# Optimization experiments

Measured on AMD Instinct MI355X. Metric: run time of the kernel, lower is better.

## Reference

```python
import jax, jax.numpy as jnp
import numpy as np

B, N, Mdim, CS, INP, OUT = 256, 2048, 64, 512, 256, 256
ADDR_R = Mdim + 6          # k(M), beta(1), g(1), s(3), gamma(1)
ADDR_W = 3 * Mdim + 6      # + erase(M) + add(M)


def setup_inputs() -> dict:
    key = jax.random.key(0)
    ks = jax.random.split(key, 16)
    s = 0.05
    x = jax.random.normal(ks[0], (B, INP), dtype=jnp.float32)
    memory = jax.random.uniform(ks[1], (B, N, Mdim), dtype=jnp.float32) * 0.1 + 1e-6
    h = jax.random.normal(ks[2], (B, CS), dtype=jnp.float32) * 0.1
    c = jax.random.normal(ks[3], (B, CS), dtype=jnp.float32) * 0.1
    rw = jax.random.uniform(ks[4], (B, N), dtype=jnp.float32)
    read_w = rw / rw.sum(axis=1, keepdims=True)
    ww = jax.random.uniform(ks[5], (B, N), dtype=jnp.float32)
    write_w = ww / ww.sum(axis=1, keepdims=True)
    prev_read = jax.random.normal(ks[6], (B, Mdim), dtype=jnp.float32) * 0.1
    W_ih = jax.random.normal(ks[7], (4 * CS, INP + Mdim), dtype=jnp.float32) * s
    W_hh = jax.random.normal(ks[8], (4 * CS, CS), dtype=jnp.float32) * s
    b_ih = jnp.zeros((4 * CS,), jnp.float32)
    b_hh = jnp.zeros((4 * CS,), jnp.float32)
    W_r = jax.random.normal(ks[9], (ADDR_R, CS), dtype=jnp.float32) * s
    b_r = jnp.zeros((ADDR_R,), jnp.float32)
    W_w = jax.random.normal(ks[10], (ADDR_W, CS), dtype=jnp.float32) * s
    b_w = jnp.zeros((ADDR_W,), jnp.float32)
    W_o = jax.random.normal(ks[11], (OUT, CS + Mdim), dtype=jnp.float32) * s
    b_o = jnp.zeros((OUT,), jnp.float32)
    return dict(x=x, memory=memory, h=h, c=c, read_w=read_w, write_w=write_w,
                prev_read=prev_read, W_ih=W_ih, W_hh=W_hh, b_ih=b_ih, b_hh=b_hh,
                W_r=W_r, b_r=b_r, W_w=W_w, b_w=b_w, W_o=W_o, b_o=b_o)


def _addressing(out_vec, prev_w, memory, M):
    # Eq. 5-9: content softmax, interpolation, circular shift, sharpening.
    k = out_vec[:, :M]                                   # [B, M]
    beta = jax.nn.softplus(out_vec[:, M:M + 1])          # [B, 1]
    g = jax.nn.sigmoid(out_vec[:, M + 1:M + 2])          # [B, 1]
    s = jax.nn.softmax(out_vec[:, M + 2:M + 5], axis=1)  # [B, 3]
    gamma = 1.0 + jax.nn.softplus(out_vec[:, M + 5:M + 6])
    norm_k = jnp.linalg.norm(k, axis=1, keepdims=True) + 1e-8        # [B, 1]
    norm_mem = jnp.linalg.norm(memory, axis=2) + 1e-8                # [B, N]
    sim = jnp.einsum('bnm,bm->bn', memory, k) / (norm_k * norm_mem)  # cosine
    w_c = jax.nn.softmax(beta * sim, axis=1)
    w_g = g * w_c + (1.0 - g) * prev_w
    # circular convolution with 3-tap shift kernel (replaces the roll loop)
    w_s = (s[:, 0:1] * jnp.roll(w_g, 1, axis=1)
           + s[:, 1:2] * w_g
           + s[:, 2:3] * jnp.roll(w_g, -1, axis=1))
    w_pow = w_s ** gamma
    return w_pow / (w_pow.sum(axis=1, keepdims=True) + 1e-8)


def reference(x, memory, h, c, read_w, write_w, prev_read,
              W_ih, W_hh, b_ih, b_hh, W_r, b_r, W_w, b_w, W_o, b_o):
    M = memory.shape[2]
    inp = jnp.concatenate([x, prev_read], axis=1)
    gates = inp @ W_ih.T + b_ih + h @ W_hh.T + b_hh
    i_g, f_g, g_g, o_g = jnp.split(gates, 4, axis=1)  # torch LSTMCell gate order
    i_g = jax.nn.sigmoid(i_g); f_g = jax.nn.sigmoid(f_g)
    g_g = jnp.tanh(g_g); o_g = jax.nn.sigmoid(o_g)
    c_new = f_g * c + i_g * g_g
    h_new = o_g * jnp.tanh(c_new)
    # read head (uses pre-write memory)
    read_out = h_new @ W_r.T + b_r
    w_read = _addressing(read_out, read_w, memory, M)
    read_vec = jnp.einsum('bn,bnm->bm', w_read, memory)
    # write head: address, then erase/add outer-product update
    write_out = h_new @ W_w.T + b_w
    w_write = _addressing(write_out, write_w, memory, M)
    erase = jax.nn.sigmoid(write_out[:, M + 6:2 * M + 6])
    add = write_out[:, 2 * M + 6:3 * M + 6]
    memory_new = memory * (1.0 - w_write[:, :, None] * erase[:, None, :]) \
                 + w_write[:, :, None] * add[:, None, :]
    out = jnp.concatenate([h_new, read_vec], axis=1) @ W_o.T + b_o
    return (out, memory_new, h_new, c_new, w_read, w_write, read_vec)
```

## Files before the change

### kernel.cpp

```cpp
#include <hip/hip_runtime.h>
#include <math.h>

#define Bsz   256
#define Nn    2048
#define Md    64
#define CSd   512
#define INPd  256
#define OUTd  256
#define KTOT  832
#define PSTRIDE 272
#define GSZ   524288

__device__ __forceinline__ float sigmoidf_(float x){ return 1.f/(1.f+expf(-x)); }
__device__ __forceinline__ float softplusf_(float x){ return fmaxf(x,0.f) + log1pf(expf(-fabsf(x))); }

__global__ __launch_bounds__(256) void k_gates(
    const float* __restrict__ x, const float* __restrict__ prev_read, const float* __restrict__ h,
    const float* __restrict__ W_ih, const float* __restrict__ W_hh,
    float* __restrict__ partials)
{
  __shared__ __align__(16) float As[16][34];
  __shared__ __align__(16) float Bs[16][68];
  const int t = threadIdx.x;
  const int col0 = blockIdx.x * 64;
  const int row0 = blockIdx.y * 32;
  const int z    = blockIdx.z;
  const int tx = t & 15;
  const int ty = t >> 4;
  const int arow = t >> 3;
  const int ak   = (t & 7) * 2;
  const int bcol = t >> 2;
  const int bk   = (t & 3) * 4;
  const int grow = row0 + arow;
  const int j    = col0 + bcol;

  float acc[2][4] = {};
  for (int kc = 0; kc < 13; ++kc) {
    const int kbase = z * 208 + kc * 16;
    #pragma unroll
    for (int i = 0; i < 2; ++i) {
      int k = kbase + ak + i;
      float v;
      if (k < INPd)            v = x[grow*INPd + k];
      else if (k < INPd+Md)    v = prev_read[grow*Md + (k-INPd)];
      else                     v = h[grow*CSd + (k-INPd-Md)];
      As[ak+i][arow] = v;
    }
    {
      int k = kbase + bk;
      float4 wv;
      if (k < INPd+Md) wv = *(const float4*)&W_ih[j*(INPd+Md) + k];
      else             wv = *(const float4*)&W_hh[j*CSd + (k-INPd-Md)];
      Bs[bk+0][bcol] = wv.x; Bs[bk+1][bcol] = wv.y;
      Bs[bk+2][bcol] = wv.z; Bs[bk+3][bcol] = wv.w;
    }
    __syncthreads();
    #pragma unroll
    for (int kk = 0; kk < 16; ++kk) {
      float2 av = *(const float2*)&As[kk][ty*2];
      float4 bv = *(const float4*)&Bs[kk][tx*4];
      acc[0][0] += av.x*bv.x; acc[0][1] += av.x*bv.y;
      acc[0][2] += av.x*bv.z; acc[0][3] += av.x*bv.w;
      acc[1][0] += av.y*bv.x; acc[1][1] += av.y*bv.y;
      acc[1][2] += av.y*bv.z; acc[1][3] += av.y*bv.w;
    }
    __syncthreads();
  }
  float* part = partials + (size_t)z * GSZ;
  #pragma unroll
  for (int i = 0; i < 2; ++i) {
    float4 v = {acc[i][0], acc[i][1], acc[i][2], acc[i][3]};
    *(float4*)&part[(row0 + ty*2 + i)*2048 + col0 + tx*4] = v;
  }
}

__global__ __launch_bounds__(256) void k_lstm(const float* __restrict__ partials,
    const float* __restrict__ c, const float* __restrict__ b_ih, const float* __restrict__ b_hh,
    float* __restrict__ h_new, float* __restrict__ c_new)
{
  int idx = blockIdx.x*256 + threadIdx.x;
  int b = idx >> 9, jj = idx & 511;
  float g[4];
  #pragma unroll
  for (int q = 0; q < 4; ++q) {
    int col = q*512 + jj;
    float s = b_ih[col] + b_hh[col];
    #pragma unroll
    for (int sp = 0; sp < 4; ++sp) s += partials[(size_t)sp*GSZ + b*2048 + col];
    g[q] = s;
  }
  float ig = sigmoidf_(g[0]);
  float fg = sigmoidf_(g[1]);
  float gg = tanhf(g[2]);
  float og = sigmoidf_(g[3]);
  float cn = fg * c[idx] + ig * gg;
  c_new[idx] = cn;
  h_new[idx] = og * tanhf(cn);
}

__global__ __launch_bounds__(512) void k_heads(
    const float* __restrict__ h_new,
    const float* __restrict__ W_r, const float* __restrict__ b_r,
    const float* __restrict__ W_w, const float* __restrict__ b_w,
    float* __restrict__ params)
{
  __shared__ float hs[CSd];
  __shared__ float ob[268];
  int b = blockIdx.x, t = threadIdx.x;
  hs[t] = h_new[b*CSd + t];
  __syncthreads();
  int wave = t >> 6, lane = t & 63;
  for (int r = wave; r < 268; r += 8) {
    const float* wrow; float bias;
    if (r < 70) { wrow = W_r + r*CSd;      bias = b_r[r]; }
    else        { wrow = W_w + (r-70)*CSd; bias = b_w[r-70]; }
    float s = 0.f;
    #pragma unroll
    for (int i = 0; i < 8; ++i) s += wrow[i*64 + lane] * hs[i*64 + lane];
    #pragma unroll
    for (int off = 32; off; off >>= 1) s += __shfl_xor(s, off);
    if (lane == 0) ob[r] = s + bias;
  }
  __syncthreads();
  float* P = params + b*PSTRIDE;
  if (t < 256) {
    if (t < 64)       P[t] = ob[t];
    else if (t < 128) P[t] = ob[70 + (t-64)];
    else if (t < 192) P[t] = sigmoidf_(ob[140 + (t-128)]);
    else              P[t] = ob[204 + (t-192)];
  }
  float* S = P + 256;
  if (wave == 0) {
    float v = ob[lane]; float sq = v*v;
    #pragma unroll
    for (int off = 32; off; off >>= 1) sq += __shfl_xor(sq, off);
    if (lane == 0) S[6] = 1.f/(sqrtf(sq)+1e-8f);
  } else if (wave == 1) {
    float v = ob[70 + lane]; float sq = v*v;
    #pragma unroll
    for (int off = 32; off; off >>= 1) sq += __shfl_xor(sq, off);
    if (lane == 0) S[13] = 1.f/(sqrtf(sq)+1e-8f);
  }
  if (t == 128) {
    S[0] = softplusf_(ob[64]);
    S[1] = sigmoidf_(ob[65]);
    float m3 = fmaxf(ob[66], fmaxf(ob[67], ob[68]));
    float e0=expf(ob[66]-m3), e1=expf(ob[67]-m3), e2=expf(ob[68]-m3);
    float es = e0+e1+e2;
    S[2]=e0/es; S[3]=e1/es; S[4]=e2/es;
    S[5] = 1.f + softplusf_(ob[69]);
  }
  if (t == 129) {
    S[7] = softplusf_(ob[134]);
    S[8] = sigmoidf_(ob[135]);
    float m3 = fmaxf(ob[136], fmaxf(ob[137], ob[138]));
    float e0=expf(ob[136]-m3), e1=expf(ob[137]-m3), e2=expf(ob[138]-m3);
    float es = e0+e1+e2;
    S[9]=e0/es; S[10]=e1/es; S[11]=e2/es;
    S[12] = 1.f + softplusf_(ob[139]);
  }
}

__global__ __launch_bounds__(256) void k_sim(
    const float* __restrict__ mem, const float* __restrict__ params,
    float* __restrict__ a_r, float* __restrict__ a_w)
{
  int b = blockIdx.y;
  int n = blockIdx.x*16 + (threadIdx.x >> 4);
  int chunk = threadIdx.x & 15;
  float4 v = ((const float4*)mem)[(b*Nn + n)*16 + chunk];
  const float* P = params + b*PSTRIDE;
  float4 kr = ((const float4*)P)[chunk];
  float4 kw = ((const float4*)(P+64))[chunk];
  float ss = v.x*v.x + v.y*v.y + v.z*v.z + v.w*v.w;
  float pr = v.x*kr.x + v.y*kr.y + v.z*kr.z + v.w*kr.w;
  float pw = v.x*kw.x + v.y*kw.y + v.z*kw.z + v.w*kw.w;
  #pragma unroll
  for (int off=8; off; off>>=1) {
    ss += __shfl_xor(ss, off);
    pr += __shfl_xor(pr, off);
    pw += __shfl_xor(pw, off);
  }
  if (chunk == 0) {
    float inv_nm = 1.f/(sqrtf(ss)+1e-8f);
    const float* S = P + 256;
    a_r[b*Nn+n] = S[0] * pr * S[6]  * inv_nm;
    a_w[b*Nn+n] = S[7] * pw * S[13] * inv_nm;
  }
}

__device__ __forceinline__ float block_reduce512(float val, float* red, int t, bool ismax){
  #pragma unroll
  for (int off=32; off; off>>=1)
    val = ismax ? fmaxf(val, __shfl_xor(val,off)) : val + __shfl_xor(val,off);
  __syncthreads();
  if ((t&63)==0) red[t>>6] = val;
  __syncthreads();
  float r = red[0];
  if (ismax) { for (int i=1;i<8;++i) r = fmaxf(r, red[i]); }
  else       { for (int i=1;i<8;++i) r += red[i]; }
  return r;
}

__global__ __launch_bounds__(512) void k_weights(
    const float* __restrict__ a_r, const float* __restrict__ a_w,
    const float* __restrict__ read_w, const float* __restrict__ write_w,
    const float* __restrict__ params,
    float* __restrict__ w_read, float* __restrict__ w_write)
{
  __shared__ float wg[Nn];
  __shared__ float red[8];
  int b = blockIdx.x;
  int which = blockIdx.y;
  const float* a    = which ? a_w     : a_r;
  const float* prev = which ? write_w : read_w;
  float* outw       = which ? w_write : w_read;
  const float* S = params + b*PSTRIDE + 256 + (which ? 7 : 0);
  float g = S[1], s0 = S[2], s1 = S[3], s2 = S[4], gamma = S[5];
  int t = threadIdx.x;
  float v[4];
  #pragma unroll
  for (int i=0;i<4;++i) v[i] = a[b*Nn + t*4+i];
  float lmax = fmaxf(fmaxf(v[0],v[1]), fmaxf(v[2],v[3]));
  float mx = block_reduce512(lmax, red, t, true);
  float e[4]; float ps = 0.f;
  #pragma unroll
  for (int i=0;i<4;++i){ e[i] = expf(v[i]-mx); ps += e[i]; }
  float denom = block_reduce512(ps, red, t, false);
  float inv = 1.f/denom;
  #pragma unroll
  for (int i=0;i<4;++i){
    float wc = e[i]*inv;
    wg[t*4+i] = g*wc + (1.f-g)*prev[b*Nn + t*4+i];
  }
  __syncthreads();
  float wp[4]; float psum = 0.f;
  #pragma unroll
  for (int i=0;i<4;++i){
    int n = t*4+i;
    float wsv = s0*wg[(n+Nn-1)&(Nn-1)] + s1*wg[n] + s2*wg[(n+1)&(Nn-1)];
    wp[i] = powf(wsv, gamma);
    psum += wp[i];
  }
  float tot = block_reduce512(psum, red, t, false);
  float invt = 1.f/(tot + 1e-8f);
  #pragma unroll
  for (int i=0;i<4;++i) outw[b*Nn + t*4+i] = wp[i]*invt;
}

__global__ __launch_bounds__(256) void k_memupd(
    const float* __restrict__ mem, const float* __restrict__ params,
    const float* __restrict__ w_read, const float* __restrict__ w_write,
    float* __restrict__ mem_new, float* __restrict__ read_vec)
{
  __shared__ __align__(16) float er[64];
  __shared__ __align__(16) float ad[64];
  __shared__ float4 part[64];
  int b = blockIdx.y;
  int n0 = blockIdx.x * 64;
  int t = threadIdx.x;
  const float* P = params + b*PSTRIDE;
  if (t < 64)       er[t]    = P[128+t];
  else if (t < 128) ad[t-64] = P[192+(t-64)];
  __syncthreads();
  int chunk = t & 15;
  int rr = t >> 4;
  float4 e4 = ((const float4*)er)[chunk];
  float4 a4 = ((const float4*)ad)[chunk];
  float4 acc = {0.f,0.f,0.f,0.f};
  #pragma unroll
  for (int p = 0; p < 4; ++p) {
    int n = n0 + p*16 + rr;
    float4 v = ((const float4*)mem)[(b*Nn+n)*16 + chunk];
    float ww = w_write[b*Nn+n];
    float wr = w_read[b*Nn+n];
    float4 o;
    o.x = v.x*(1.f-ww*e4.x) + ww*a4.x;
    o.y = v.y*(1.f-ww*e4.y) + ww*a4.y;
    o.z = v.z*(1.f-ww*e4.z) + ww*a4.z;
    o.w = v.w*(1.f-ww*e4.w) + ww*a4.w;
    ((float4*)mem_new)[(b*Nn+n)*16 + chunk] = o;
    acc.x += wr*v.x; acc.y += wr*v.y; acc.z += wr*v.z; acc.w += wr*v.w;
  }
  #pragma unroll
  for (int off = 16; off <= 32; off <<= 1) {
    acc.x += __shfl_xor(acc.x, off);
    acc.y += __shfl_xor(acc.y, off);
    acc.z += __shfl_xor(acc.z, off);
    acc.w += __shfl_xor(acc.w, off);
  }
  int wave = t >> 6;
  int lane = t & 63;
  if (lane < 16) part[wave*16 + chunk] = acc;
  __syncthreads();
  if (t < 16) {
    float4 s = part[t];
    for (int w=1; w<4; ++w){ float4 q = part[w*16+t]; s.x+=q.x; s.y+=q.y; s.z+=q.z; s.w+=q.w; }
    atomicAdd(&read_vec[b*64 + t*4+0], s.x);
    atomicAdd(&read_vec[b*64 + t*4+1], s.y);
    atomicAdd(&read_vec[b*64 + t*4+2], s.z);
    atomicAdd(&read_vec[b*64 + t*4+3], s.w);
  }
}

__global__ __launch_bounds__(256) void k_out(
    const float* __restrict__ h_new, const float* __restrict__ read_vec,
    const float* __restrict__ W_o, const float* __restrict__ b_o,
    float* __restrict__ out)
{
  __shared__ float vbuf[576];
  int b = blockIdx.y, t = threadIdx.x;
  vbuf[t]     = h_new[b*CSd + t];
  vbuf[t+256] = h_new[b*CSd + t + 256];
  if (t < 64) vbuf[512+t] = read_vec[b*64 + t];
  __syncthreads();
  int wave = t >> 6, lane = t & 63;
  float vb[9];
  #pragma unroll
  for (int i = 0; i < 9; ++i) vb[i] = vbuf[i*64 + lane];
  int cbase = blockIdx.x*64 + wave*16;
  for (int jj = 0; jj < 16; ++jj) {
    int cc = cbase + jj;
    const float* w = W_o + cc*576;
    float s = 0.f;
    #pragma unroll
    for (int i = 0; i < 9; ++i) s += w[i*64 + lane] * vb[i];
    #pragma unroll
    for (int off = 32; off; off >>= 1) s += __shfl_xor(s, off);
    if (lane == 0) out[b*OUTd + cc] = s + b_o[cc];
  }
}

extern "C" void kernel_launch(void* const* d_in, const int* in_sizes, int n_in,
                              void* d_out, int out_size, void* d_ws, size_t ws_size,
                              hipStream_t stream)
{
  const float* x         = (const float*)d_in[0];
  const float* memory    = (const float*)d_in[1];
  const float* h         = (const float*)d_in[2];
  const float* c         = (const float*)d_in[3];
  const float* read_w    = (const float*)d_in[4];
  const float* write_w   = (const float*)d_in[5];
  const float* prev_read = (const float*)d_in[6];
  const float* W_ih      = (const float*)d_in[7];
  const float* W_hh      = (const float*)d_in[8];
  const float* b_ih      = (const float*)d_in[9];
  const float* b_hh      = (const float*)d_in[10];
  const float* W_r       = (const float*)d_in[11];
  const float* b_r       = (const float*)d_in[12];
  const float* W_w       = (const float*)d_in[13];
  const float* b_w       = (const float*)d_in[14];
  const float* W_o       = (const float*)d_in[15];
  const float* b_o       = (const float*)d_in[16];

  float* out      = (float*)d_out;
  float* mem_new  = out + 256*256;
  float* h_new    = mem_new + (size_t)256*2048*64;
  float* c_new    = h_new + 256*512;
  float* w_read   = c_new + 256*512;
  float* w_write  = w_read + 256*2048;
  float* read_vec = w_write + 256*2048;

  float* ws       = (float*)d_ws;
  float* params   = ws;
  float* partials = params + 256*PSTRIDE;
  float* a_r      = partials;
  float* a_w      = partials + GSZ;

  k_gates  <<<dim3(32,8,4), 256, 0, stream>>>(x, prev_read, h, W_ih, W_hh, partials);
  k_lstm   <<<512,          256, 0, stream>>>(partials, c, b_ih, b_hh, h_new, c_new);
  k_heads  <<<256,          512, 0, stream>>>(h_new, W_r, b_r, W_w, b_w, params);
  k_sim    <<<dim3(128,256),256, 0, stream>>>(memory, params, a_r, a_w);
  k_weights<<<dim3(256,2),  512, 0, stream>>>(a_r, a_w, read_w, write_w, params, w_read, w_write);
  hipMemsetAsync(read_vec, 0, 256*64*sizeof(float), stream);
  k_memupd <<<dim3(32,256), 256, 0, stream>>>(memory, params, w_read, w_write, mem_new, read_vec);
  k_out    <<<dim3(4,256),  256, 0, stream>>>(h_new, read_vec, W_o, b_o, out);
}
```

Measured before the change: 376.0 us.

## Retile gates GEMM, fuse LSTM with heads, replace read-vector atomics with partials

The gates GEMM now uses 64-thread blocks, each computing an 8x8 register tile per thread over a 64x64 output tile. It splits K eight ways and prefetches the next K slice into registers while the current one is being multiplied. The LSTM cell update is fused into the head-projection kernel, so h_new goes straight to shared memory and one launch plus a global round trip disappears. The read-vector atomics and their memset are replaced by per-block partial sums that k_out reduces. The cost is more workspace for eight split-K partials, and the fused kernel has to sum eight partials per gate.

```diff
diff --git a/kernel.cpp b/kernel.cpp
--- a/kernel.cpp
+++ b/kernel.cpp
@@ -10,104 +10,110 @@
 #define KTOT  832
 #define PSTRIDE 272
 #define GSZ   524288
+#define ZSPL  8
+#define KZ    104
 
 __device__ __forceinline__ float sigmoidf_(float x){ return 1.f/(1.f+expf(-x)); }
 __device__ __forceinline__ float softplusf_(float x){ return fmaxf(x,0.f) + log1pf(expf(-fabsf(x))); }
 
-__global__ __launch_bounds__(256) void k_gates(
+__device__ __forceinline__ float4 loadA4(const float* __restrict__ x, const float* __restrict__ pr,
+                                         const float* __restrict__ h, int row, int k){
+  if (k < INPd)            return *(const float4*)&x[row*INPd + k];
+  else if (k < INPd+Md)    return *(const float4*)&pr[row*Md + (k-INPd)];
+  else                     return *(const float4*)&h[row*CSd + (k-INPd-Md)];
+}
+__device__ __forceinline__ float4 loadW4(const float* __restrict__ Wih, const float* __restrict__ Whh,
+                                         int j, int k){
+  if (k < INPd+Md)         return *(const float4*)&Wih[j*(INPd+Md) + k];
+  else                     return *(const float4*)&Whh[j*CSd + (k-INPd-Md)];
+}
+
+__global__ __launch_bounds__(64) void k_gates(
     const float* __restrict__ x, const float* __restrict__ prev_read, const float* __restrict__ h,
     const float* __restrict__ W_ih, const float* __restrict__ W_hh,
     float* __restrict__ partials)
 {
-  __shared__ __align__(16) float As[16][34];
-  __shared__ __align__(16) float Bs[16][68];
+  __shared__ __align__(16) float As[8][68];
+  __shared__ __align__(16) float Bs[8][68];
   const int t = threadIdx.x;
   const int col0 = blockIdx.x * 64;
-  const int row0 = blockIdx.y * 32;
+  const int row0 = blockIdx.y * 64;
   const int z    = blockIdx.z;
-  const int tx = t & 15;
-  const int ty = t >> 4;
-  const int arow = t >> 3;
-  const int ak   = (t & 7) * 2;
-  const int bcol = t >> 2;
-  const int bk   = (t & 3) * 4;
-  const int grow = row0 + arow;
-  const int j    = col0 + bcol;
-
-  float acc[2][4] = {};
+  const int tr = t >> 3, tc = t & 7;
+  const int row = row0 + t;
+  const int j   = col0 + t;
+
+  float acc[8][8] = {};
+  float4 a0, a1, b0, b1;
+  int kb = z * KZ;
+  a0 = loadA4(x, prev_read, h, row, kb);   a1 = loadA4(x, prev_read, h, row, kb+4);
+  b0 = loadW4(W_ih, W_hh, j, kb);          b1 = loadW4(W_ih, W_hh, j, kb+4);
+
   for (int kc = 0; kc < 13; ++kc) {
-    const int kbase = z * 208 + kc * 16;
-    #pragma unroll
-    for (int i = 0; i < 2; ++i) {
-      int k = kbase + ak + i;
-      float v;
-      if (k < INPd)            v = x[grow*INPd + k];
-      else if (k < INPd+Md)    v = prev_read[grow*Md + (k-INPd)];
-      else                     v = h[grow*CSd + (k-INPd-Md)];
-      As[ak+i][arow] = v;
+    As[0][t]=a0.x; As[1][t]=a0.y; As[2][t]=a0.z; As[3][t]=a0.w;
+    As[4][t]=a1.x; As[5][t]=a1.y; As[6][t]=a1.z; As[7][t]=a1.w;
+    Bs[0][t]=b0.x; Bs[1][t]=b0.y; Bs[2][t]=b0.z; Bs[3][t]=b0.w;
+    Bs[4][t]=b1.x; Bs[5][t]=b1.y; Bs[6][t]=b1.z; Bs[7][t]=b1.w;
+    __syncthreads();
+    if (kc < 12) {
+      int kn = kb + (kc+1)*8;
+      a0 = loadA4(x, prev_read, h, row, kn);   a1 = loadA4(x, prev_read, h, row, kn+4);
+      b0 = loadW4(W_ih, W_hh, j, kn);          b1 = loadW4(W_ih, W_hh, j, kn+4);
     }
-    {
-      int k = kbase + bk;
-      float4 wv;
-      if (k < INPd+Md) wv = *(const float4*)&W_ih[j*(INPd+Md) + k];
-      else             wv = *(const float4*)&W_hh[j*CSd + (k-INPd-Md)];
-      Bs[bk+0][bcol] = wv.x; Bs[bk+1][bcol] = wv.y;
-      Bs[bk+2][bcol] = wv.z; Bs[bk+3][bcol] = wv.w;
+    #pragma unroll
+    for (int kk = 0; kk < 8; ++kk) {
+      float av[8], bv[8];
+      *(float4*)&av[0] = *(const float4*)&As[kk][tr*8];
+      *(float4*)&av[4] = *(const float4*)&As[kk][tr*8+4];
+      *(float4*)&bv[0] = *(const float4*)&Bs[kk][tc*8];
+      *(float4*)&bv[4] = *(const float4*)&Bs[kk][tc*8+4];
+      #pragma unroll
+      for (int i=0;i<8;++i)
+        #pragma unroll
+        for (int q=0;q<8;++q)
+          acc[i][q] += av[i]*bv[q];
     }
     __syncthreads();
-    #pragma unroll
-    for (int kk = 0; kk < 16; ++kk) {
-      float2 av = *(const float2*)&As[kk][ty*2];
-      float4 bv = *(const float4*)&Bs[kk][tx*4];
-      acc[0][0] += av.x*bv.x; acc[0][1] += av.x*bv.y;
-      acc[0][2] += av.x*bv.z; acc[0][3] += av.x*bv.w;
-      acc[1][0] += av.y*bv.x; acc[1][1] += av.y*bv.y;
-      acc[1][2] += av.y*bv.z; acc[1][3] += av.y*bv.w;
-    }
-    __syncthreads();
   }
   float* part = partials + (size_t)z * GSZ;
   #pragma unroll
-  for (int i = 0; i < 2; ++i) {
-    float4 v = {acc[i][0], acc[i][1], acc[i][2], acc[i][3]};
-    *(float4*)&part[(row0 + ty*2 + i)*2048 + col0 + tx*4] = v;
-  }
-}
-
-__global__ __launch_bounds__(256) void k_lstm(const float* __restrict__ partials,
-    const float* __restrict__ c, const float* __restrict__ b_ih, const float* __restrict__ b_hh,
-    float* __restrict__ h_new, float* __restrict__ c_new)
-{
-  int idx = blockIdx.x*256 + threadIdx.x;
-  int b = idx >> 9, jj = idx & 511;
+  for (int i=0;i<8;++i) {
+    int r = row0 + tr*8 + i;
+    float4 v0 = {acc[i][0],acc[i][1],acc[i][2],acc[i][3]};
+    float4 v1 = {acc[i][4],acc[i][5],acc[i][6],acc[i][7]};
+    *(float4*)&part[r*2048 + col0 + tc*8]     = v0;
+    *(float4*)&part[r*2048 + col0 + tc*8 + 4] = v1;
+  }
+}
+
+__global__ __launch_bounds__(512) void k_lstm_heads(
+    const float* __restrict__ partials, const float* __restrict__ c,
+    const float* __restrict__ b_ih, const float* __restrict__ b_hh,
+    const float* __restrict__ W_r, const float* __restrict__ b_r,
+    const float* __restrict__ W_w, const float* __restrict__ b_w,
+    float* __restrict__ h_new, float* __restrict__ c_new, float* __restrict__ params)
+{
+  __shared__ float hs[CSd];
+  __shared__ float ob[268];
+  int b = blockIdx.x, t = threadIdx.x;
   float g[4];
   #pragma unroll
   for (int q = 0; q < 4; ++q) {
-    int col = q*512 + jj;
+    int col = q*512 + t;
     float s = b_ih[col] + b_hh[col];
     #pragma unroll
-    for (int sp = 0; sp < 4; ++sp) s += partials[(size_t)sp*GSZ + b*2048 + col];
+    for (int sp = 0; sp < ZSPL; ++sp) s += partials[(size_t)sp*GSZ + b*2048 + col];
     g[q] = s;
   }
   float ig = sigmoidf_(g[0]);
   float fg = sigmoidf_(g[1]);
   float gg = tanhf(g[2]);
   float og = sigmoidf_(g[3]);
-  float cn = fg * c[idx] + ig * gg;
-  c_new[idx] = cn;
-  h_new[idx] = og * tanhf(cn);
-}
-
-__global__ __launch_bounds__(512) void k_heads(
-    const float* __restrict__ h_new,
-    const float* __restrict__ W_r, const float* __restrict__ b_r,
-    const float* __restrict__ W_w, const float* __restrict__ b_w,
-    float* __restrict__ params)
-{
-  __shared__ float hs[CSd];
-  __shared__ float ob[268];
-  int b = blockIdx.x, t = threadIdx.x;
-  hs[t] = h_new[b*CSd + t];
+  float cn = fg * c[b*CSd + t] + ig * gg;
+  float hn = og * tanhf(cn);
+  c_new[b*CSd + t] = cn;
+  h_new[b*CSd + t] = hn;
+  hs[t] = hn;
   __syncthreads();
   int wave = t >> 6, lane = t & 63;
   for (int r = wave; r < 268; r += 8) {
@@ -251,7 +257,7 @@
 __global__ __launch_bounds__(256) void k_memupd(
     const float* __restrict__ mem, const float* __restrict__ params,
     const float* __restrict__ w_read, const float* __restrict__ w_write,
-    float* __restrict__ mem_new, float* __restrict__ read_vec)
+    float* __restrict__ mem_new, float* __restrict__ prv)
 {
   __shared__ __align__(16) float er[64];
   __shared__ __align__(16) float ad[64];
@@ -290,29 +296,31 @@
     acc.w += __shfl_xor(acc.w, off);
   }
   int wave = t >> 6;
-  int lane = t & 63;
-  if (lane < 16) part[wave*16 + chunk] = acc;
+  if ((t & 63) < 16) part[wave*16 + chunk] = acc;
   __syncthreads();
   if (t < 16) {
     float4 s = part[t];
     for (int w=1; w<4; ++w){ float4 q = part[w*16+t]; s.x+=q.x; s.y+=q.y; s.z+=q.z; s.w+=q.w; }
-    atomicAdd(&read_vec[b*64 + t*4+0], s.x);
-    atomicAdd(&read_vec[b*64 + t*4+1], s.y);
-    atomicAdd(&read_vec[b*64 + t*4+2], s.z);
-    atomicAdd(&read_vec[b*64 + t*4+3], s.w);
+    *(float4*)&prv[(b*32 + blockIdx.x)*64 + t*4] = s;
   }
 }
 
 __global__ __launch_bounds__(256) void k_out(
-    const float* __restrict__ h_new, const float* __restrict__ read_vec,
+    const float* __restrict__ h_new, const float* __restrict__ prv,
     const float* __restrict__ W_o, const float* __restrict__ b_o,
-    float* __restrict__ out)
+    float* __restrict__ out, float* __restrict__ read_vec)
 {
   __shared__ float vbuf[576];
   int b = blockIdx.y, t = threadIdx.x;
   vbuf[t]     = h_new[b*CSd + t];
   vbuf[t+256] = h_new[b*CSd + t + 256];
-  if (t < 64) vbuf[512+t] = read_vec[b*64 + t];
+  if (t < 64) {
+    float s = 0.f;
+    #pragma unroll 8
+    for (int i = 0; i < 32; ++i) s += prv[(b*32 + i)*64 + t];
+    vbuf[512+t] = s;
+    if (blockIdx.x == 0) read_vec[b*64 + t] = s;
+  }
   __syncthreads();
   int wave = t >> 6, lane = t & 63;
   float vb[9];
@@ -366,13 +374,13 @@
   float* partials = params + 256*PSTRIDE;
   float* a_r      = partials;
   float* a_w      = partials + GSZ;
-
-  k_gates  <<<dim3(32,8,4), 256, 0, stream>>>(x, prev_read, h, W_ih, W_hh, partials);
-  k_lstm   <<<512,          256, 0, stream>>>(partials, c, b_ih, b_hh, h_new, c_new);
-  k_heads  <<<256,          512, 0, stream>>>(h_new, W_r, b_r, W_w, b_w, params);
-  k_sim    <<<dim3(128,256),256, 0, stream>>>(memory, params, a_r, a_w);
-  k_weights<<<dim3(256,2),  512, 0, stream>>>(a_r, a_w, read_w, write_w, params, w_read, w_write);
-  hipMemsetAsync(read_vec, 0, 256*64*sizeof(float), stream);
-  k_memupd <<<dim3(32,256), 256, 0, stream>>>(memory, params, w_read, w_write, mem_new, read_vec);
-  k_out    <<<dim3(4,256),  256, 0, stream>>>(h_new, read_vec, W_o, b_o, out);
-}
+  float* prv      = partials + 2*GSZ;
+
+  k_gates     <<<dim3(32,4,ZSPL), 64, 0, stream>>>(x, prev_read, h, W_ih, W_hh, partials);
+  k_lstm_heads<<<256,            512, 0, stream>>>(partials, c, b_ih, b_hh, W_r, b_r, W_w, b_w,
+                                                   h_new, c_new, params);
+  k_sim       <<<dim3(128,256),  256, 0, stream>>>(memory, params, a_r, a_w);
+  k_weights   <<<dim3(256,2),    512, 0, stream>>>(a_r, a_w, read_w, write_w, params, w_read, w_write);
+  k_memupd    <<<dim3(32,256),   256, 0, stream>>>(memory, params, w_read, w_write, mem_new, prv);
+  k_out       <<<dim3(4,256),    256, 0, stream>>>(h_new, prv, W_o, b_o, out, read_vec);
+}
```

After: 369.3 us. Within noise of the previous version (-1.8%).
